# Kernel tuning notes

Hardware: AMD Instinct MI355X
Metric: run time of the kernel (lower is better)

Reference implementation:

```python
import jax, jax.numpy as jnp
import numpy as np

N_NODES = 50000
N_EDGES = 800000
IN_C = 128
HID = 64
HEADS = 4
OUT_C = 32
NEG_SLOPE = 0.2
EPS = 1e-16


def _gat_conv(x, edge_index, W, att_src, att_dst, bias, heads, out_c, concat):
    # PyG GATConv (eval mode, add_self_loops=True).
    N = x.shape[0]
    # append self loops
    loops = jnp.arange(N, dtype=edge_index.dtype)
    src = jnp.concatenate([edge_index[0], loops])
    dst = jnp.concatenate([edge_index[1], loops])
    h = (x @ W).reshape(N, heads, out_c)                      # [N,H,C]
    a_src = jnp.sum(h * att_src, axis=-1)                     # [N,H]
    a_dst = jnp.sum(h * att_dst, axis=-1)                     # [N,H]
    alpha = a_src[src] + a_dst[dst]                           # [E,H]
    alpha = jnp.where(alpha >= 0, alpha, NEG_SLOPE * alpha)   # leaky_relu
    amax = jax.ops.segment_max(alpha, dst, num_segments=N)    # [N,H]
    ex = jnp.exp(alpha - amax[dst])
    denom = jax.ops.segment_sum(ex, dst, num_segments=N)      # [N,H]
    coef = ex / (denom[dst] + EPS)                            # [E,H]
    msg = h[src] * coef[:, :, None]                           # [E,H,C]
    out = jax.ops.segment_sum(msg, dst, num_segments=N)       # [N,H,C]
    if concat:
        out = out.reshape(N, heads * out_c)
    else:
        out = out.mean(axis=1)
    return out + bias


def setup_inputs() -> dict:
    key = jax.random.key(0)
    ks = jax.random.split(key, 12)
    x = jax.random.normal(ks[0], (N_NODES, IN_C), dtype=jnp.float32)
    edge_index = jax.random.randint(ks[1], (2, N_EDGES), 0, N_NODES, dtype=jnp.int64)
    s1 = 1.0 / np.sqrt(IN_C)
    s2 = 1.0 / np.sqrt(HID * HEADS)
    W1 = jax.random.uniform(ks[2], (IN_C, HEADS * HID), jnp.float32, -s1, s1)
    att_src1 = jax.random.uniform(ks[3], (HEADS, HID), jnp.float32, -s1, s1)
    att_dst1 = jax.random.uniform(ks[4], (HEADS, HID), jnp.float32, -s1, s1)
    b1 = jnp.zeros((HEADS * HID,), jnp.float32)
    W2 = jax.random.uniform(ks[5], (HEADS * HID, OUT_C), jnp.float32, -s2, s2)
    att_src2 = jax.random.uniform(ks[6], (1, OUT_C), jnp.float32, -s2, s2)
    att_dst2 = jax.random.uniform(ks[7], (1, OUT_C), jnp.float32, -s2, s2)
    b2 = jnp.zeros((OUT_C,), jnp.float32)
    return {"x": x, "edge_index": edge_index, "W1": W1, "att_src1": att_src1,
            "att_dst1": att_dst1, "b1": b1, "W2": W2, "att_src2": att_src2,
            "att_dst2": att_dst2, "b2": b2}


def reference(x, edge_index, W1, att_src1, att_dst1, b1, W2, att_src2, att_dst2, b2):
    h = _gat_conv(x, edge_index, W1, att_src1, att_dst1, b1, HEADS, HID, concat=True)
    h = jax.nn.elu(h)
    out = _gat_conv(h, edge_index, W2, att_src2, att_dst2, b2, 1, OUT_C, concat=False)
    return out
```

## Files before the change

kernel.cpp:

```cpp
#include <hip/hip_runtime.h>

#define NN 50000
#define NE 800000
#define INC 128
#define HIDC 64
#define HEADS 4
#define C1 256
#define OUTC 32
#define NEG 0.2f
#define EPSV 1e-16f
#define SLOT_CAP 56
#define CSTRIDE 16

#define NB_CASTX 3125
#define NB_ZERO  3125
#define NB_W1T   128
#define NB_W2T   32
#define NB_PREP  (NB_CASTX + NB_ZERO + NB_W1T + NB_W2T)
#define EB2      3125
#define NB_G1S   782
#define NB_G1    (NB_G1S * 4)
#define NB_GS    (EB2 + NB_G1)

#define CURS  0
#define ASRC1 800000
#define ADST1 1000000
#define ASRC2 1200000
#define ADST2 1250000
#define SLOTS 1300000
#define W1T   4100000
#define W2T   4116384
#define XBF   4120480
#define H1B   7320480
#define H2B   13720480
#define H3OFF 20120480
#define WS_NEED_FLOATS 20920480ull

typedef __attribute__((ext_vector_type(8))) short short8v;
typedef __attribute__((ext_vector_type(4))) float floatx4;

__device__ __forceinline__ unsigned short f2bf(float f) {
    unsigned u = __float_as_uint(f);
    unsigned r = (u + 0x7fffu + ((u >> 16) & 1u)) >> 16;
    return (unsigned short)r;
}
__device__ __forceinline__ float bf2f(unsigned short s) {
    return __uint_as_float(((unsigned)s) << 16);
}
__device__ __forceinline__ float lrelu(float v) { return v >= 0.f ? v : NEG * v; }

__global__ __launch_bounds__(256) void prep(const float* __restrict__ x,
                                            const float* __restrict__ W1,
                                            const float* __restrict__ W2,
                                            unsigned short* __restrict__ xbf,
                                            unsigned short* __restrict__ w1t,
                                            unsigned short* __restrict__ w2t,
                                            int* __restrict__ curs) {
    const int bid = blockIdx.x, tid = threadIdx.x;
    if (bid < NB_CASTX) {
        int i = bid * 256 + tid;
        float4 v0 = ((const float4*)x)[i * 2];
        float4 v1 = ((const float4*)x)[i * 2 + 1];
        short8v o;
        o[0] = (short)f2bf(v0.x); o[1] = (short)f2bf(v0.y);
        o[2] = (short)f2bf(v0.z); o[3] = (short)f2bf(v0.w);
        o[4] = (short)f2bf(v1.x); o[5] = (short)f2bf(v1.y);
        o[6] = (short)f2bf(v1.z); o[7] = (short)f2bf(v1.w);
        *(short8v*)(xbf + (size_t)i * 8) = o;
    } else if (bid < NB_CASTX + NB_ZERO) {
        int i = (bid - NB_CASTX) * 256 + tid;
        curs[i] = 0;
    } else if (bid < NB_CASTX + NB_ZERO + NB_W1T) {
        int i = (bid - NB_CASTX - NB_ZERO) * 256 + tid;
        int n = i >> 7, k = i & 127;
        w1t[(size_t)n * INC + k] = f2bf(W1[(size_t)k * C1 + n]);
    } else {
        int i = (bid - NB_CASTX - NB_ZERO - NB_W1T) * 256 + tid;
        int n = i >> 8, k = i & 255;
        w2t[(size_t)n * C1 + k] = f2bf(W2[(size_t)k * OUTC + n]);
    }
}

__global__ __launch_bounds__(256) void gemm1_scatter(const unsigned short* __restrict__ xbf,
                                                     const unsigned short* __restrict__ w1t,
                                                     const float* __restrict__ att_src,
                                                     const float* __restrict__ att_dst,
                                                     const int* __restrict__ ei,
                                                     unsigned short* __restrict__ h1b,
                                                     float* __restrict__ a_src,
                                                     float* __restrict__ a_dst,
                                                     int* __restrict__ curs,
                                                     int* __restrict__ slots) {
    const int bid = blockIdx.x;
    if (bid < EB2) {
        int e = bid * 256 + threadIdx.x;
        if (e < NE) {
            int s = ei[e], d = ei[NE + e];
            int pos = atomicAdd(&curs[d * CSTRIDE], 1);
            if (pos < SLOT_CAP) slots[(size_t)d * SLOT_CAP + pos] = s;
        }
        return;
    }
    const int b2 = bid - EB2;
    const int strip = b2 % NB_G1S;
    const int by = b2 / NB_G1S;
    const int tid = threadIdx.x;
    const int w = tid >> 6, lane = tid & 63;
    const int l15 = lane & 15, kg = lane >> 4;
    const int mb = strip * 64 + w * 16;
    const int nb = by * 64;
    int ar = mb + l15; if (ar >= NN) ar = NN - 1;

    short8v a[4];
    #pragma unroll
    for (int ks = 0; ks < 4; ++ks)
        a[ks] = *(const short8v*)(xbf + (size_t)ar * INC + ks * 32 + kg * 8);

    short8v b[4][4];
    #pragma unroll
    for (int nt = 0; nt < 4; ++nt) {
        int nc = nb + nt * 16 + l15;
        #pragma unroll
        for (int ks = 0; ks < 4; ++ks)
            b[ks][nt] = *(const short8v*)(w1t + (size_t)nc * INC + ks * 32 + kg * 8);
    }

    floatx4 acc[4] = {{0.f,0.f,0.f,0.f},{0.f,0.f,0.f,0.f},{0.f,0.f,0.f,0.f},{0.f,0.f,0.f,0.f}};
    #pragma unroll
    for (int ks = 0; ks < 4; ++ks)
        #pragma unroll
        for (int nt = 0; nt < 4; ++nt)
            acc[nt] = __builtin_amdgcn_mfma_f32_16x16x32_bf16(a[ks], b[ks][nt], acc[nt], 0, 0, 0);

    #pragma unroll
    for (int nt = 0; nt < 4; ++nt)
        #pragma unroll
        for (int j = 0; j < 4; ++j) {
            int r = mb + kg * 4 + j;
            if (r < NN) h1b[(size_t)r * C1 + nb + nt * 16 + l15] = f2bf(acc[nt][j]);
        }

    float ws_[4], wd_[4];
    #pragma unroll
    for (int nt = 0; nt < 4; ++nt) {
        ws_[nt] = att_src[nb + nt * 16 + l15];
        wd_[nt] = att_dst[nb + nt * 16 + l15];
    }
    #pragma unroll
    for (int j = 0; j < 4; ++j) {
        float ps = acc[0][j] * ws_[0] + acc[1][j] * ws_[1] + acc[2][j] * ws_[2] + acc[3][j] * ws_[3];
        float pd = acc[0][j] * wd_[0] + acc[1][j] * wd_[1] + acc[2][j] * wd_[2] + acc[3][j] * wd_[3];
        #pragma unroll
        for (int m = 8; m; m >>= 1) {
            ps += __shfl_xor(ps, m);
            pd += __shfl_xor(pd, m);
        }
        int r = mb + kg * 4 + j;
        if (l15 == 0 && r < NN) {
            a_src[r * 4 + by] = ps;
            a_dst[r * 4 + by] = pd;
        }
    }
}

__global__ __launch_bounds__(256) void node1(const unsigned short* __restrict__ h1b,
                                             const int* __restrict__ curs,
                                             const int* __restrict__ slots,
                                             const float* __restrict__ a_src,
                                             const float* __restrict__ a_dst,
                                             const float* __restrict__ b1,
                                             unsigned short* __restrict__ h2b) {
    int wave = threadIdx.x >> 6, lane = threadIdx.x & 63;
    int n = blockIdx.x * 4 + wave;
    if (n >= NN) return;
    int h = lane >> 4;
    int cnt = curs[n * CSTRIDE]; if (cnt > SLOT_CAP) cnt = SLOT_CAP;
    const int* sl = slots + (size_t)n * SLOT_CAP;
    float adh = a_dst[n * 4 + h];
    float a0 = 0.f, a1 = 0.f, a2 = 0.f, a3 = 0.f, den = 0.f;
    {
        float e = __expf(lrelu(a_src[n * 4 + h] + adh));
        den += e;
        uint2 rv = *(const uint2*)(h1b + (size_t)n * C1 + lane * 4);
        a0 += bf2f((unsigned short)(rv.x & 0xffff)) * e;
        a1 += bf2f((unsigned short)(rv.x >> 16)) * e;
        a2 += bf2f((unsigned short)(rv.y & 0xffff)) * e;
        a3 += bf2f((unsigned short)(rv.y >> 16)) * e;
    }
    int p = 0;
    for (; p + 7 < cnt; p += 8) {
        int sA[8];
        #pragma unroll
        for (int j = 0; j < 8; ++j) sA[j] = sl[p + j];
        uint2 rA[8];
        #pragma unroll
        for (int j = 0; j < 8; ++j) rA[j] = *(const uint2*)(h1b + (size_t)sA[j] * C1 + lane * 4);
        float eA[8];
        #pragma unroll
        for (int j = 0; j < 8; ++j) eA[j] = __expf(lrelu(a_src[sA[j] * 4 + h] + adh));
        #pragma unroll
        for (int j = 0; j < 8; ++j) {
            den += eA[j];
            a0 += bf2f((unsigned short)(rA[j].x & 0xffff)) * eA[j];
            a1 += bf2f((unsigned short)(rA[j].x >> 16)) * eA[j];
            a2 += bf2f((unsigned short)(rA[j].y & 0xffff)) * eA[j];
            a3 += bf2f((unsigned short)(rA[j].y >> 16)) * eA[j];
        }
    }
    for (; p + 3 < cnt; p += 4) {
        int sA[4];
        #pragma unroll
        for (int j = 0; j < 4; ++j) sA[j] = sl[p + j];
        uint2 rA[4];
        #pragma unroll
        for (int j = 0; j < 4; ++j) rA[j] = *(const uint2*)(h1b + (size_t)sA[j] * C1 + lane * 4);
        float eA[4];
        #pragma unroll
        for (int j = 0; j < 4; ++j) eA[j] = __expf(lrelu(a_src[sA[j] * 4 + h] + adh));
        #pragma unroll
        for (int j = 0; j < 4; ++j) {
            den += eA[j];
            a0 += bf2f((unsigned short)(rA[j].x & 0xffff)) * eA[j];
            a1 += bf2f((unsigned short)(rA[j].x >> 16)) * eA[j];
            a2 += bf2f((unsigned short)(rA[j].y & 0xffff)) * eA[j];
            a3 += bf2f((unsigned short)(rA[j].y >> 16)) * eA[j];
        }
    }
    for (; p < cnt; ++p) {
        int s = sl[p];
        float e = __expf(lrelu(a_src[s * 4 + h] + adh));
        den += e;
        uint2 rv = *(const uint2*)(h1b + (size_t)s * C1 + lane * 4);
        a0 += bf2f((unsigned short)(rv.x & 0xffff)) * e;
        a1 += bf2f((unsigned short)(rv.x >> 16)) * e;
        a2 += bf2f((unsigned short)(rv.y & 0xffff)) * e;
        a3 += bf2f((unsigned short)(rv.y >> 16)) * e;
    }
    float inv = 1.f / (den + EPSV);
    float4 bb = *(const float4*)(b1 + lane * 4);
    float o0 = a0 * inv + bb.x;
    float o1 = a1 * inv + bb.y;
    float o2 = a2 * inv + bb.z;
    float o3 = a3 * inv + bb.w;
    o0 = o0 > 0.f ? o0 : __expf(o0) - 1.f;
    o1 = o1 > 0.f ? o1 : __expf(o1) - 1.f;
    o2 = o2 > 0.f ? o2 : __expf(o2) - 1.f;
    o3 = o3 > 0.f ? o3 : __expf(o3) - 1.f;
    uint2 ov;
    ov.x = (unsigned)f2bf(o0) | ((unsigned)f2bf(o1) << 16);
    ov.y = (unsigned)f2bf(o2) | ((unsigned)f2bf(o3) << 16);
    *(uint2*)(h2b + (size_t)n * C1 + lane * 4) = ov;
}

__global__ __launch_bounds__(256) void gemm2_mfma(const unsigned short* __restrict__ h2b,
                                                  const unsigned short* __restrict__ w2t,
                                                  const float* __restrict__ att_src,
                                                  const float* __restrict__ att_dst,
                                                  unsigned short* __restrict__ h3b,
                                                  float* __restrict__ a_src,
                                                  float* __restrict__ a_dst) {
    const int tid = threadIdx.x;
    const int w = tid >> 6, lane = tid & 63;
    const int l15 = lane & 15, kg = lane >> 4;
    const int mb = blockIdx.x * 64 + w * 16;
    int ar = mb + l15; if (ar >= NN) ar = NN - 1;

    short8v a[8];
    #pragma unroll
    for (int ks = 0; ks < 8; ++ks)
        a[ks] = *(const short8v*)(h2b + (size_t)ar * C1 + ks * 32 + kg * 8);

    short8v b[8][2];
    #pragma unroll
    for (int nt = 0; nt < 2; ++nt) {
        int nc = nt * 16 + l15;
        #pragma unroll
        for (int ks = 0; ks < 8; ++ks)
            b[ks][nt] = *(const short8v*)(w2t + (size_t)nc * C1 + ks * 32 + kg * 8);
    }

    floatx4 acc[2] = {{0.f,0.f,0.f,0.f},{0.f,0.f,0.f,0.f}};
    #pragma unroll
    for (int ks = 0; ks < 8; ++ks)
        #pragma unroll
        for (int nt = 0; nt < 2; ++nt)
            acc[nt] = __builtin_amdgcn_mfma_f32_16x16x32_bf16(a[ks], b[ks][nt], acc[nt], 0, 0, 0);

    #pragma unroll
    for (int nt = 0; nt < 2; ++nt)
        #pragma unroll
        for (int j = 0; j < 4; ++j) {
            int r = mb + kg * 4 + j;
            if (r < NN) h3b[(size_t)r * OUTC + nt * 16 + l15] = f2bf(acc[nt][j]);
        }

    float ws0 = att_src[l15], ws1 = att_src[16 + l15];
    float wd0 = att_dst[l15], wd1 = att_dst[16 + l15];
    #pragma unroll
    for (int j = 0; j < 4; ++j) {
        float ps = acc[0][j] * ws0 + acc[1][j] * ws1;
        float pd = acc[0][j] * wd0 + acc[1][j] * wd1;
        #pragma unroll
        for (int m = 8; m; m >>= 1) {
            ps += __shfl_xor(ps, m);
            pd += __shfl_xor(pd, m);
        }
        int r = mb + kg * 4 + j;
        if (l15 == 0 && r < NN) {
            a_src[r] = ps;
            a_dst[r] = pd;
        }
    }
}

__global__ __launch_bounds__(256) void node2(const unsigned short* __restrict__ h3b,
                                             const int* __restrict__ curs,
                                             const int* __restrict__ slots,
                                             const float* __restrict__ a_src,
                                             const float* __restrict__ a_dst,
                                             const float* __restrict__ b2,
                                             float* __restrict__ out) {
    int wave = threadIdx.x >> 6, lane = threadIdx.x & 63;
    int half = lane >> 5, c = lane & 31;
    int n = blockIdx.x * 8 + wave * 2 + half;
    if (n >= NN) return;
    int cnt = curs[n * CSTRIDE]; if (cnt > SLOT_CAP) cnt = SLOT_CAP;
    const int* sl = slots + (size_t)n * SLOT_CAP;
    float adn = a_dst[n];
    float acc = 0.f, den = 0.f;
    {
        float e = __expf(lrelu(a_src[n] + adn));
        den += e;
        acc += bf2f(h3b[(size_t)n * OUTC + c]) * e;
    }
    int p = 0;
    for (; p + 3 < cnt; p += 4) {
        int s0 = sl[p], s1 = sl[p + 1], s2 = sl[p + 2], s3 = sl[p + 3];
        float g0 = bf2f(h3b[(size_t)s0 * OUTC + c]);
        float g1 = bf2f(h3b[(size_t)s1 * OUTC + c]);
        float g2 = bf2f(h3b[(size_t)s2 * OUTC + c]);
        float g3 = bf2f(h3b[(size_t)s3 * OUTC + c]);
        float e0 = __expf(lrelu(a_src[s0] + adn));
        float e1 = __expf(lrelu(a_src[s1] + adn));
        float e2 = __expf(lrelu(a_src[s2] + adn));
        float e3 = __expf(lrelu(a_src[s3] + adn));
        den += e0 + e1 + e2 + e3;
        acc += g0 * e0 + g1 * e1 + g2 * e2 + g3 * e3;
    }
    for (; p < cnt; ++p) {
        int s = sl[p];
        float e = __expf(lrelu(a_src[s] + adn));
        den += e;
        acc += bf2f(h3b[(size_t)s * OUTC + c]) * e;
    }
    out[(size_t)n * OUTC + c] = acc / (den + EPSV) + b2[c];
}

extern "C" void kernel_launch(void* const* d_in, const int* in_sizes, int n_in,
                              void* d_out, int out_size, void* d_ws, size_t ws_size,
                              hipStream_t stream) {
    if (ws_size < WS_NEED_FLOATS * 4ull) return;

    const float* x        = (const float*)d_in[0];
    const int* ei         = (const int*)d_in[1];
    const float* W1       = (const float*)d_in[2];
    const float* att_src1 = (const float*)d_in[3];
    const float* att_dst1 = (const float*)d_in[4];
    const float* b1       = (const float*)d_in[5];
    const float* W2       = (const float*)d_in[6];
    const float* att_src2 = (const float*)d_in[7];
    const float* att_dst2 = (const float*)d_in[8];
    const float* b2       = (const float*)d_in[9];
    float* out = (float*)d_out;
    float* ws  = (float*)d_ws;
    int*   wsi = (int*)d_ws;

    int*   curs   = wsi + CURS;
    float* a_src1 = ws + ASRC1;
    float* a_dst1 = ws + ADST1;
    float* a_src2 = ws + ASRC2;
    float* a_dst2 = ws + ADST2;
    int*   slots  = wsi + SLOTS;
    unsigned short* w1t = (unsigned short*)(ws + W1T);
    unsigned short* w2t = (unsigned short*)(ws + W2T);
    unsigned short* xbf = (unsigned short*)(ws + XBF);
    unsigned short* h1b = (unsigned short*)(ws + H1B);
    unsigned short* h2b = (unsigned short*)(ws + H2B);
    unsigned short* h3b = (unsigned short*)(ws + H3OFF);

    hipLaunchKernelGGL(prep, dim3(NB_PREP), dim3(256), 0, stream,
                       x, W1, W2, xbf, w1t, w2t, curs);
    hipLaunchKernelGGL(gemm1_scatter, dim3(NB_GS), dim3(256), 0, stream,
                       xbf, w1t, att_src1, att_dst1, ei, h1b, a_src1, a_dst1, curs, slots);
    hipLaunchKernelGGL(node1, dim3((NN + 3) / 4), dim3(256), 0, stream,
                       h1b, curs, slots, a_src1, a_dst1, b1, h2b);
    hipLaunchKernelGGL(gemm2_mfma, dim3((NN + 63) / 64), dim3(256), 0, stream,
                       h2b, w2t, att_src2, att_dst2, h3b, a_src2, a_dst2);
    hipLaunchKernelGGL(node2, dim3((NN + 7) / 8), dim3(256), 0, stream,
                       h3b, curs, slots, a_src2, a_dst2, b2, out);
}
```

Before: 189.9 us.

## Compute all four heads per block and stage h1 output through LDS

The GEMM part of the fused scatter/gemm kernel now has each block compute all 256 output columns for its 64-row strip instead of one 64-column head slice, cutting that grid by four and reusing the loaded x fragments across heads. Results are staged in a 32 KB shared tile and written back as coalesced 16-byte row stores instead of scattered 2-byte stores. The cost is more serial work per block, fewer blocks, and shared memory use that may lower occupancy.

```diff
diff --git a/kernel.cpp b/kernel.cpp
--- a/kernel.cpp
+++ b/kernel.cpp
@@ -19,8 +19,7 @@
 #define NB_PREP  (NB_CASTX + NB_ZERO + NB_W1T + NB_W2T)
 #define EB2      3125
 #define NB_G1S   782
-#define NB_G1    (NB_G1S * 4)
-#define NB_GS    (EB2 + NB_G1)
+#define NB_GS    (EB2 + NB_G1S)
 
 #define CURS  0
 #define ASRC1 800000
@@ -101,14 +100,12 @@
         }
         return;
     }
+    __shared__ unsigned short tile[4][16][256];
     const int b2 = bid - EB2;
-    const int strip = b2 % NB_G1S;
-    const int by = b2 / NB_G1S;
     const int tid = threadIdx.x;
     const int w = tid >> 6, lane = tid & 63;
     const int l15 = lane & 15, kg = lane >> 4;
-    const int mb = strip * 64 + w * 16;
-    const int nb = by * 64;
+    const int mb = b2 * 64 + w * 16;
     int ar = mb + l15; if (ar >= NN) ar = NN - 1;
 
     short8v a[4];
@@ -116,49 +113,61 @@
     for (int ks = 0; ks < 4; ++ks)
         a[ks] = *(const short8v*)(xbf + (size_t)ar * INC + ks * 32 + kg * 8);
 
-    short8v b[4][4];
-    #pragma unroll
-    for (int nt = 0; nt < 4; ++nt) {
-        int nc = nb + nt * 16 + l15;
+    #pragma unroll
+    for (int hh = 0; hh < 4; ++hh) {
+        const int nb = hh * 64;
+        short8v b[4][4];
+        #pragma unroll
+        for (int nt = 0; nt < 4; ++nt) {
+            int nc = nb + nt * 16 + l15;
+            #pragma unroll
+            for (int ks = 0; ks < 4; ++ks)
+                b[ks][nt] = *(const short8v*)(w1t + (size_t)nc * INC + ks * 32 + kg * 8);
+        }
+        floatx4 acc[4] = {{0.f,0.f,0.f,0.f},{0.f,0.f,0.f,0.f},{0.f,0.f,0.f,0.f},{0.f,0.f,0.f,0.f}};
         #pragma unroll
         for (int ks = 0; ks < 4; ++ks)
-            b[ks][nt] = *(const short8v*)(w1t + (size_t)nc * INC + ks * 32 + kg * 8);
-    }
-
-    floatx4 acc[4] = {{0.f,0.f,0.f,0.f},{0.f,0.f,0.f,0.f},{0.f,0.f,0.f,0.f},{0.f,0.f,0.f,0.f}};
-    #pragma unroll
-    for (int ks = 0; ks < 4; ++ks)
+            #pragma unroll
+            for (int nt = 0; nt < 4; ++nt)
+                acc[nt] = __builtin_amdgcn_mfma_f32_16x16x32_bf16(a[ks], b[ks][nt], acc[nt], 0, 0, 0);
+
         #pragma unroll
         for (int nt = 0; nt < 4; ++nt)
-            acc[nt] = __builtin_amdgcn_mfma_f32_16x16x32_bf16(a[ks], b[ks][nt], acc[nt], 0, 0, 0);
-
-    #pragma unroll
-    for (int nt = 0; nt < 4; ++nt)
+            #pragma unroll
+            for (int j = 0; j < 4; ++j)
+                tile[w][kg * 4 + j][nb + nt * 16 + l15] = f2bf(acc[nt][j]);
+
+        float ws_[4], wd_[4];
+        #pragma unroll
+        for (int nt = 0; nt < 4; ++nt) {
+            ws_[nt] = att_src[nb + nt * 16 + l15];
+            wd_[nt] = att_dst[nb + nt * 16 + l15];
+        }
         #pragma unroll
         for (int j = 0; j < 4; ++j) {
+            float ps = acc[0][j] * ws_[0] + acc[1][j] * ws_[1] + acc[2][j] * ws_[2] + acc[3][j] * ws_[3];
+            float pd = acc[0][j] * wd_[0] + acc[1][j] * wd_[1] + acc[2][j] * wd_[2] + acc[3][j] * wd_[3];
+            #pragma unroll
+            for (int m = 8; m; m >>= 1) {
+                ps += __shfl_xor(ps, m);
+                pd += __shfl_xor(pd, m);
+            }
             int r = mb + kg * 4 + j;
-            if (r < NN) h1b[(size_t)r * C1 + nb + nt * 16 + l15] = f2bf(acc[nt][j]);
-        }
-
-    float ws_[4], wd_[4];
-    #pragma unroll
-    for (int nt = 0; nt < 4; ++nt) {
-        ws_[nt] = att_src[nb + nt * 16 + l15];
-        wd_[nt] = att_dst[nb + nt * 16 + l15];
-    }
-    #pragma unroll
-    for (int j = 0; j < 4; ++j) {
-        float ps = acc[0][j] * ws_[0] + acc[1][j] * ws_[1] + acc[2][j] * ws_[2] + acc[3][j] * ws_[3];
-        float pd = acc[0][j] * wd_[0] + acc[1][j] * wd_[1] + acc[2][j] * wd_[2] + acc[3][j] * wd_[3];
-        #pragma unroll
-        for (int m = 8; m; m >>= 1) {
-            ps += __shfl_xor(ps, m);
-            pd += __shfl_xor(pd, m);
-        }
-        int r = mb + kg * 4 + j;
-        if (l15 == 0 && r < NN) {
-            a_src[r * 4 + by] = ps;
-            a_dst[r * 4 + by] = pd;
+            if (l15 == 0 && r < NN) {
+                a_src[r * 4 + hh] = ps;
+                a_dst[r * 4 + hh] = pd;
+            }
+        }
+    }
+    __syncthreads();
+    #pragma unroll
+    for (int pass = 0; pass < 8; ++pass) {
+        int row = pass * 2 + (lane >> 5);
+        int slot = lane & 31;
+        int r = mb + row;
+        if (r < NN) {
+            uint4 v = *(const uint4*)&tile[w][row][slot * 8];
+            *(uint4*)(h1b + (size_t)r * C1 + slot * 8) = v;
         }
     }
 }
```

Result: slower. 206.2 us (+8.6%).
